# Kernel tuning notes

Hardware: AMD Instinct MI355X
Metric: run time of the kernel (lower is better)

Reference implementation:

```python
import jax, jax.numpy as jnp
import numpy as np

DK = 64  # embedding_size / h = 1024 / 16


def setup_inputs() -> dict:
    key = jax.random.key(0)
    k1, k2, k3 = jax.random.split(key, 3)
    S = 8192
    return {
        "q": jax.random.normal(k1, (S, DK), dtype=jnp.float32),
        "k": jax.random.normal(k2, (S, DK), dtype=jnp.float32),
        "v": jax.random.normal(k3, (S, DK), dtype=jnp.float32),
    }


def reference(q, k, v):
    # scores: [S, S]; NOTE: source scales by 1/dk (not 1/sqrt(dk)) — kept faithful.
    qk = jnp.matmul(q, k.T) * (1.0 / DK)
    S = qk.shape[0]
    # causal mask: position (i, j) allowed iff i >= j (0 added), else -inf
    i = jnp.arange(S)[:, None]
    j = jnp.arange(S)[None, :]
    qk = jnp.where(i >= j, qk, -jnp.inf)
    attn = jax.nn.softmax(qk, axis=-1)
    return jnp.matmul(attn, v)
```

## Files before the change

### kernel.cpp

```cpp
#include <hip/hip_runtime.h>
#include <hip/hip_bf16.h>

#define S_LEN 8192
#define DKD   64
#define BM    64
#define BN    64
#define PAD   8
#define LDK   (DKD + PAD)

#define CHUNK 512
#define NC    (S_LEN / CHUNK)
#define NWORK 1088

#define WS_NEED ((size_t)2 * S_LEN * DKD * 2 + (size_t)NC * S_LEN * 4 + (size_t)NC * S_LEN * DKD * 2)

typedef __bf16 bf16x8 __attribute__((ext_vector_type(8)));
typedef float  f32x4  __attribute__((ext_vector_type(4)));
typedef unsigned short ushort8v __attribute__((ext_vector_type(8)));
typedef unsigned short ushort4v __attribute__((ext_vector_type(4)));

__device__ __forceinline__ unsigned short f2bf(float f) {
  union { float f; unsigned u; } v; v.f = f;
  unsigned u = v.u;
  return (unsigned short)((u + 0x7fffu + ((u >> 16) & 1u)) >> 16);
}
__device__ __forceinline__ float bf2f(unsigned short s) {
  union { unsigned u; float f; } v; v.u = ((unsigned)s) << 16;
  return v.f;
}
__device__ __forceinline__ unsigned pk2(float a, float b) {
  union { float f; unsigned u; } x, y; x.f = a; y.f = b;
  return ((x.u + 0x8000u) >> 16) | ((y.u + 0x8000u) & 0xffff0000u);
}
__device__ __forceinline__ bf16x8 q_frag8(const float* p, float sc) {
  float4 u = *(const float4*)p;
  float4 w = *(const float4*)(p + 4);
  union { ushort8v s; bf16x8 b; } r;
  r.s[0] = f2bf(u.x * sc); r.s[1] = f2bf(u.y * sc);
  r.s[2] = f2bf(u.z * sc); r.s[3] = f2bf(u.w * sc);
  r.s[4] = f2bf(w.x * sc); r.s[5] = f2bf(w.y * sc);
  r.s[6] = f2bf(w.z * sc); r.s[7] = f2bf(w.w * sc);
  return r.b;
}

__global__ __launch_bounds__(256) void precompute(const float* __restrict__ k,
                                                  const float* __restrict__ v,
                                                  unsigned short* __restrict__ Ff) {
  __shared__ unsigned short Ls[64][72];
  const int b = blockIdx.x, tid = threadIdx.x;
  unsigned short* tb = Ff + ((size_t)b << 13);

#pragma unroll
  for (int j = 0; j < 4; ++j) {
    int vi = tid + j * 256;
    int row = vi >> 4, c4 = vi & 15;
    float4 x = *(const float4*)(v + ((size_t)(b * 64 + row)) * DKD + c4 * 4);
    Ls[row][c4 * 4 + 0] = f2bf(x.x);
    Ls[row][c4 * 4 + 1] = f2bf(x.y);
    Ls[row][c4 * 4 + 2] = f2bf(x.z);
    Ls[row][c4 * 4 + 3] = f2bf(x.w);
  }

#pragma unroll
  for (int j = 0; j < 2; ++j) {
    int idx = tid + j * 256;
    int f = idx >> 6, lane = idx & 63;
    int col = lane & 15, quad = lane >> 4;
    int t = f >> 1, c = f & 1;
    const float* src = k + ((size_t)(b * 64 + 16 * t + col)) * DKD + c * 32 + quad * 8;
    union { ushort8v s; bf16x8 bb; } r;
    r.bb = q_frag8(src, 1.0f);
    *(ushort8v*)(tb + (size_t)(f * 64 + lane) * 8) = r.s;
  }
  __syncthreads();

#pragma unroll
  for (int j = 0; j < 2; ++j) {
    int idx = tid + j * 256;
    int f8 = idx >> 6, lane = idx & 63;
    int col = lane & 15, quad = lane >> 4;
    int dt = f8 >> 1, c = f8 & 1;
    int d = 16 * dt + col;
    ushort8v o;
#pragma unroll
    for (int j2 = 0; j2 < 8; ++j2) {
      int kk = c * 32 + quad * 8 + j2;
      int s = (((kk & 7) >> 2) + 2 * (kk >> 5)) * 16 + (((kk >> 3) & 3) << 2) + (kk & 3);
      o[j2] = Ls[s][d];
    }
    *(ushort8v*)(tb + (size_t)((8 + f8) * 64 + lane) * 8) = o;
  }
}

__global__ __launch_bounds__(256) void attn_partial(const float* __restrict__ qg,
                                                    const unsigned short* __restrict__ Ff,
                                                    unsigned short* __restrict__ Opart,
                                                    float* __restrict__ l_ws) {
  const int w = blockIdx.x;
  int g = (int)((sqrtf((float)w + 1.0f) - 1.0f) * 0.5f);
  while (4 * (g + 1) * (g + 2) <= w) ++g;
  while (4 * g * (g + 1) > w) --g;
  const int r0  = w - 4 * g * (g + 1);
  const int qq  = r0 / (g + 1);
  const int qt  = 8 * g + qq;
  const int cch = r0 - qq * (g + 1);

  const int q0 = qt * BM, chunk0 = cch * CHUNK;
  const int n_kt = min(CHUNK / BN, qt - 8 * cch + 1);
  const int tile0 = chunk0 >> 6;

  const int tid = threadIdx.x, wave = tid >> 6, lane = tid & 63;
  const int col = lane & 15, quad = lane >> 4;

  const int qidx = q0 + wave * 16 + col;
  const float* qp = qg + (size_t)qidx * DKD;
  bf16x8 b0 = q_frag8(qp + quad * 8, 1.0f / 64.0f);
  bf16x8 b1 = q_frag8(qp + 32 + quad * 8, 1.0f / 64.0f);

  float lsum = 0.0f;
  f32x4 Of[4];
#pragma unroll
  for (int i = 0; i < 4; ++i) Of[i] = f32x4{0.0f, 0.0f, 0.0f, 0.0f};

  for (int it = 0; it < n_kt; ++it) {
    const unsigned short* tb = Ff + ((size_t)(tile0 + it) << 13);
    const int k0 = chunk0 + it * BN;

    bf16x8 kf[8];
#pragma unroll
    for (int f = 0; f < 8; ++f)
      kf[f] = *(const bf16x8*)(tb + (size_t)((f << 6) + lane) * 8);

    f32x4 Sf[4];
#pragma unroll
    for (int t = 0; t < 4; ++t) {
      f32x4 acc = f32x4{0.0f, 0.0f, 0.0f, 0.0f};
      acc = __builtin_amdgcn_mfma_f32_16x16x32_bf16(kf[2 * t], b0, acc, 0, 0, 0);
      acc = __builtin_amdgcn_mfma_f32_16x16x32_bf16(kf[2 * t + 1], b1, acc, 0, 0, 0);
      Sf[t] = acc;
    }

    bf16x8 vf[8];
#pragma unroll
    for (int f = 0; f < 8; ++f)
      vf[f] = *(const bf16x8*)(tb + (size_t)(((8 + f) << 6) + lane) * 8);

#pragma unroll
    for (int t = 0; t < 4; ++t) {
      int kb = k0 + t * 16 + quad * 4;
#pragma unroll
      for (int r = 0; r < 4; ++r) {
        float p = __expf(Sf[t][r]);
        p = (kb + r <= qidx) ? p : 0.0f;
        Sf[t][r] = p;
        lsum += p;
      }
    }

    union { unsigned u[4]; bf16x8 b; } pa0, pa1;
    pa0.u[0] = pk2(Sf[0][0], Sf[0][1]); pa0.u[1] = pk2(Sf[0][2], Sf[0][3]);
    pa0.u[2] = pk2(Sf[1][0], Sf[1][1]); pa0.u[3] = pk2(Sf[1][2], Sf[1][3]);
    pa1.u[0] = pk2(Sf[2][0], Sf[2][1]); pa1.u[1] = pk2(Sf[2][2], Sf[2][3]);
    pa1.u[2] = pk2(Sf[3][0], Sf[3][1]); pa1.u[3] = pk2(Sf[3][2], Sf[3][3]);

#pragma unroll
    for (int dt = 0; dt < 4; ++dt) {
      Of[dt] = __builtin_amdgcn_mfma_f32_16x16x32_bf16(pa0.b, vf[2 * dt], Of[dt], 0, 0, 0);
      Of[dt] = __builtin_amdgcn_mfma_f32_16x16x32_bf16(pa1.b, vf[2 * dt + 1], Of[dt], 0, 0, 0);
    }
  }

  lsum += __shfl_xor(lsum, 16);
  lsum += __shfl_xor(lsum, 32);
  if (lane < 16)
    l_ws[cch * S_LEN + q0 + wave * 16 + lane] = lsum;

#pragma unroll
  for (int r = 0; r < 4; ++r) {
    int rowg = q0 + wave * 16 + quad * 4 + r;
    uint2 o2;
    o2.x = pk2(Of[0][r], Of[1][r]);
    o2.y = pk2(Of[2][r], Of[3][r]);
    *(uint2*)(Opart + ((size_t)cch * S_LEN + rowg) * DKD + col * 4) = o2;
  }
}

__global__ __launch_bounds__(256) void attn_merge(const unsigned short* __restrict__ Opart,
                                                  const float* __restrict__ l_ws,
                                                  float* __restrict__ out) {
  int idx = blockIdx.x * 256 + threadIdx.x;
  int row = idx >> 3, m = idx & 7;
  int nc = (row >> 9) + 1;

  float acc[8] = {0, 0, 0, 0, 0, 0, 0, 0};
  float L = 0.0f;
  for (int c = 0; c < nc; ++c) {
    L += l_ws[c * S_LEN + row];
    ushort8v o = *(const ushort8v*)(Opart + ((size_t)c * S_LEN + row) * DKD + m * 8);
#pragma unroll
    for (int j = 0; j < 8; ++j) acc[j] += bf2f(o[j]);
  }
  float inv = 1.0f / L;
#pragma unroll
  for (int j0 = 0; j0 < 4; ++j0) {
    float2 w2 = { acc[j0] * inv, acc[j0 + 4] * inv };
    *(float2*)(out + (size_t)row * DKD + 16 * j0 + 2 * m) = w2;
  }
}

__global__ __launch_bounds__(128) void attn_fwd(const float* __restrict__ qg,
                                                const float* __restrict__ kg,
                                                const float* __restrict__ vg,
                                                float* __restrict__ out) {
  __shared__ __align__(16) unsigned short Qs[32][LDK];
  __shared__ __align__(16) unsigned short Ksh[BN][LDK];
  __shared__ __align__(16) unsigned short Vt[DKD][LDK];
  __shared__ __align__(16) unsigned short Ps[2][16][LDK];

  const int tid = threadIdx.x, wave = tid >> 6, lane = tid & 63;
  const int col = lane & 15, quad = lane >> 4;
  const int q0 = blockIdx.x * 32;

#pragma unroll
  for (int r = 0; r < 4; ++r) {
    int vi = tid + r * 128;
    int row = vi >> 4, c4 = vi & 15;
    if (row < 32) {
      float4 val = *(const float4*)(qg + (size_t)(q0 + row) * DKD + c4 * 4);
      Qs[row][c4 * 4 + 0] = f2bf(val.x);
      Qs[row][c4 * 4 + 1] = f2bf(val.y);
      Qs[row][c4 * 4 + 2] = f2bf(val.z);
      Qs[row][c4 * 4 + 3] = f2bf(val.w);
    }
  }

  float m_run[4], l_run[4];
  f32x4 Of[4];
#pragma unroll
  for (int i = 0; i < 4; ++i) {
    m_run[i] = -1e30f; l_run[i] = 0.0f;
    Of[i] = f32x4{0.0f, 0.0f, 0.0f, 0.0f};
  }

  const int n_tiles = (q0 + 31) / BN + 1;
  for (int it = 0; it < n_tiles; ++it) {
    __syncthreads();
    const int k0 = it * BN;
#pragma unroll
    for (int r = 0; r < 8; ++r) {
      int vi = tid + r * 128;
      int row = vi >> 4, c4 = vi & 15;
      float4 kv = *(const float4*)(kg + (size_t)(k0 + row) * DKD + c4 * 4);
      Ksh[row][c4 * 4 + 0] = f2bf(kv.x);
      Ksh[row][c4 * 4 + 1] = f2bf(kv.y);
      Ksh[row][c4 * 4 + 2] = f2bf(kv.z);
      Ksh[row][c4 * 4 + 3] = f2bf(kv.w);
      float4 vv = *(const float4*)(vg + (size_t)(k0 + row) * DKD + c4 * 4);
      Vt[c4 * 4 + 0][row] = f2bf(vv.x);
      Vt[c4 * 4 + 1][row] = f2bf(vv.y);
      Vt[c4 * 4 + 2][row] = f2bf(vv.z);
      Vt[c4 * 4 + 3][row] = f2bf(vv.w);
    }
    __syncthreads();

    f32x4 Sf[4];
    const unsigned short* qrow = &Qs[wave * 16 + col][0];
#pragma unroll
    for (int t = 0; t < 4; ++t) {
      f32x4 acc = f32x4{0.0f, 0.0f, 0.0f, 0.0f};
#pragma unroll
      for (int c = 0; c < 2; ++c) {
        bf16x8 a = *(const bf16x8*)(qrow + c * 32 + quad * 8);
        bf16x8 b = *(const bf16x8*)(&Ksh[t * 16 + col][c * 32 + quad * 8]);
        acc = __builtin_amdgcn_mfma_f32_16x16x32_bf16(a, b, acc, 0, 0, 0);
      }
      Sf[t] = acc;
    }

    const float scale = 1.0f / 64.0f;
    float rmax[4] = {-1e30f, -1e30f, -1e30f, -1e30f};
#pragma unroll
    for (int t = 0; t < 4; ++t) {
      int kidx = k0 + t * 16 + col;
#pragma unroll
      for (int r = 0; r < 4; ++r) {
        int qidx = q0 + wave * 16 + quad * 4 + r;
        float s = Sf[t][r] * scale;
        s = (kidx <= qidx) ? s : -1e30f;
        Sf[t][r] = s;
        rmax[r] = fmaxf(rmax[r], s);
      }
    }
#pragma unroll
    for (int off = 1; off <= 8; off <<= 1)
#pragma unroll
      for (int r = 0; r < 4; ++r)
        rmax[r] = fmaxf(rmax[r], __shfl_xor(rmax[r], off));

    float alpha[4], rsum[4];
#pragma unroll
    for (int r = 0; r < 4; ++r) {
      float mn = fmaxf(m_run[r], rmax[r]);
      alpha[r] = __expf(m_run[r] - mn);
      m_run[r] = mn;
      rsum[r] = 0.0f;
    }
#pragma unroll
    for (int t = 0; t < 4; ++t)
#pragma unroll
      for (int r = 0; r < 4; ++r) {
        float p = __expf(Sf[t][r] - m_run[r]);
        Sf[t][r] = p;
        rsum[r] += p;
      }
#pragma unroll
    for (int off = 1; off <= 8; off <<= 1)
#pragma unroll
      for (int r = 0; r < 4; ++r)
        rsum[r] += __shfl_xor(rsum[r], off);
#pragma unroll
    for (int r = 0; r < 4; ++r)
      l_run[r] = l_run[r] * alpha[r] + rsum[r];
#pragma unroll
    for (int dt = 0; dt < 4; ++dt)
#pragma unroll
      for (int r = 0; r < 4; ++r)
        Of[dt][r] *= alpha[r];

#pragma unroll
    for (int t = 0; t < 4; ++t)
#pragma unroll
      for (int r = 0; r < 4; ++r)
        Ps[wave][quad * 4 + r][t * 16 + col] = f2bf(Sf[t][r]);
    __syncthreads();

    const unsigned short* prow = &Ps[wave][col][0];
#pragma unroll
    for (int dt = 0; dt < 4; ++dt) {
#pragma unroll
      for (int c = 0; c < 2; ++c) {
        bf16x8 a = *(const bf16x8*)(prow + c * 32 + quad * 8);
        bf16x8 b = *(const bf16x8*)(&Vt[dt * 16 + col][c * 32 + quad * 8]);
        Of[dt] = __builtin_amdgcn_mfma_f32_16x16x32_bf16(a, b, Of[dt], 0, 0, 0);
      }
    }
  }

#pragma unroll
  for (int r = 0; r < 4; ++r) {
    float inv = 1.0f / l_run[r];
    int qrow_g = q0 + wave * 16 + quad * 4 + r;
#pragma unroll
    for (int dt = 0; dt < 4; ++dt)
      out[(size_t)qrow_g * DKD + dt * 16 + col] = Of[dt][r] * inv;
  }
}

extern "C" void kernel_launch(void* const* d_in, const int* in_sizes, int n_in,
                              void* d_out, int out_size, void* d_ws, size_t ws_size,
                              hipStream_t stream) {
  const float* q = (const float*)d_in[0];
  const float* k = (const float*)d_in[1];
  const float* v = (const float*)d_in[2];
  float* out = (float*)d_out;

  if (ws_size >= WS_NEED) {
    unsigned short* Ff    = (unsigned short*)d_ws;
    float* l_ws           = (float*)(Ff + (size_t)2 * S_LEN * DKD);
    unsigned short* Opart = (unsigned short*)(l_ws + (size_t)NC * S_LEN);

    hipLaunchKernelGGL(precompute, dim3(S_LEN / 64), dim3(256), 0, stream, k, v, Ff);
    hipLaunchKernelGGL(attn_partial, dim3(NWORK), dim3(256), 0, stream,
                       q, Ff, Opart, l_ws);
    hipLaunchKernelGGL(attn_merge, dim3(S_LEN * 8 / 256), dim3(256), 0, stream,
                       Opart, l_ws, out);
  } else {
    hipLaunchKernelGGL(attn_fwd, dim3(S_LEN / 32), dim3(128), 0, stream, q, k, v, out);
  }
}
```

Before: 94.79 us.

## Double query tile per block and stage K/V tiles through LDS with async loads

```diff
diff --git a/kernel.cpp b/kernel.cpp
--- a/kernel.cpp
+++ b/kernel.cpp
@@ -3,14 +3,14 @@
 
 #define S_LEN 8192
 #define DKD   64
-#define BM    64
+#define BM    128
 #define BN    64
 #define PAD   8
 #define LDK   (DKD + PAD)
 
 #define CHUNK 512
 #define NC    (S_LEN / CHUNK)
-#define NWORK 1088
+#define NWORK 544
 
 #define WS_NEED ((size_t)2 * S_LEN * DKD * 2 + (size_t)NC * S_LEN * 4 + (size_t)NC * S_LEN * DKD * 2)
 
@@ -18,6 +18,9 @@
 typedef float  f32x4  __attribute__((ext_vector_type(4)));
 typedef unsigned short ushort8v __attribute__((ext_vector_type(8)));
 typedef unsigned short ushort4v __attribute__((ext_vector_type(4)));
+
+typedef __attribute__((address_space(3))) unsigned int lds_uint;
+typedef const __attribute__((address_space(1))) unsigned int glb_uint;
 
 __device__ __forceinline__ unsigned short f2bf(float f) {
   union { float f; unsigned u; } v; v.f = f;
@@ -92,96 +95,143 @@
   }
 }
 
+__device__ __forceinline__ void stage_tile(const unsigned short* tb,
+                                           unsigned short* dst,
+                                           int wave) {
+#pragma unroll
+  for (int p = 0; p < 4; ++p) {
+    const int seg = p * 4 + wave;
+    __builtin_amdgcn_global_load_lds(
+        (glb_uint*)(tb + ((size_t)seg << 9) + (size_t)(threadIdx.x & 63) * 8),
+        (lds_uint*)(dst + ((size_t)seg << 9)),
+        16, 0, 0);
+  }
+}
+
 __global__ __launch_bounds__(256) void attn_partial(const float* __restrict__ qg,
                                                     const unsigned short* __restrict__ Ff,
                                                     unsigned short* __restrict__ Opart,
                                                     float* __restrict__ l_ws) {
-  const int w = blockIdx.x;
-  int g = (int)((sqrtf((float)w + 1.0f) - 1.0f) * 0.5f);
-  while (4 * (g + 1) * (g + 2) <= w) ++g;
-  while (4 * g * (g + 1) > w) --g;
-  const int r0  = w - 4 * g * (g + 1);
+  const int wr = (NWORK - 1) - blockIdx.x;
+  int g = (int)((sqrtf(2.0f * wr + 1.0f) - 1.0f) * 0.5f);
+  while (2 * (g + 1) * (g + 2) <= wr) ++g;
+  while (2 * g * (g + 1) > wr) --g;
+  const int r0  = wr - 2 * g * (g + 1);
   const int qq  = r0 / (g + 1);
-  const int qt  = 8 * g + qq;
+  const int qt  = 4 * g + qq;
   const int cch = r0 - qq * (g + 1);
 
   const int q0 = qt * BM, chunk0 = cch * CHUNK;
-  const int n_kt = min(CHUNK / BN, qt - 8 * cch + 1);
-  const int tile0 = chunk0 >> 6;
+  const int n_kt = min(CHUNK / BN, 2 * qt + 2 - 8 * cch);
+  const int tile0 = cch * 8;
+
+  __shared__ __align__(16) unsigned short Buf[2][8192];
 
   const int tid = threadIdx.x, wave = tid >> 6, lane = tid & 63;
   const int col = lane & 15, quad = lane >> 4;
 
-  const int qidx = q0 + wave * 16 + col;
-  const float* qp = qg + (size_t)qidx * DKD;
-  bf16x8 b0 = q_frag8(qp + quad * 8, 1.0f / 64.0f);
-  bf16x8 b1 = q_frag8(qp + 32 + quad * 8, 1.0f / 64.0f);
-
-  float lsum = 0.0f;
-  f32x4 Of[4];
-#pragma unroll
-  for (int i = 0; i < 4; ++i) Of[i] = f32x4{0.0f, 0.0f, 0.0f, 0.0f};
+  const int base0 = q0 + wave * 32;
+  const int qi0 = base0 + col, qi1 = base0 + 16 + col;
+  bf16x8 b0g0 = q_frag8(qg + (size_t)qi0 * DKD + quad * 8, 1.0f / 64.0f);
+  bf16x8 b1g0 = q_frag8(qg + (size_t)qi0 * DKD + 32 + quad * 8, 1.0f / 64.0f);
+  bf16x8 b0g1 = q_frag8(qg + (size_t)qi1 * DKD + quad * 8, 1.0f / 64.0f);
+  bf16x8 b1g1 = q_frag8(qg + (size_t)qi1 * DKD + 32 + quad * 8, 1.0f / 64.0f);
+
+  float ls0 = 0.0f, ls1 = 0.0f;
+  f32x4 Of0[4], Of1[4];
+#pragma unroll
+  for (int i = 0; i < 4; ++i) {
+    Of0[i] = f32x4{0.0f, 0.0f, 0.0f, 0.0f};
+    Of1[i] = f32x4{0.0f, 0.0f, 0.0f, 0.0f};
+  }
+
+  stage_tile(Ff + ((size_t)tile0 << 13), &Buf[0][0], wave);
+  __syncthreads();
 
   for (int it = 0; it < n_kt; ++it) {
-    const unsigned short* tb = Ff + ((size_t)(tile0 + it) << 13);
+    if (it + 1 < n_kt)
+      stage_tile(Ff + ((size_t)(tile0 + it + 1) << 13), &Buf[(it + 1) & 1][0], wave);
+
+    const unsigned short* B = &Buf[it & 1][0];
     const int k0 = chunk0 + it * BN;
 
     bf16x8 kf[8];
 #pragma unroll
     for (int f = 0; f < 8; ++f)
-      kf[f] = *(const bf16x8*)(tb + (size_t)((f << 6) + lane) * 8);
-
-    f32x4 Sf[4];
+      kf[f] = *(const bf16x8*)(B + (size_t)((f << 6) + lane) * 8);
+
+    f32x4 S0[4], S1[4];
 #pragma unroll
     for (int t = 0; t < 4; ++t) {
-      f32x4 acc = f32x4{0.0f, 0.0f, 0.0f, 0.0f};
-      acc = __builtin_amdgcn_mfma_f32_16x16x32_bf16(kf[2 * t], b0, acc, 0, 0, 0);
-      acc = __builtin_amdgcn_mfma_f32_16x16x32_bf16(kf[2 * t + 1], b1, acc, 0, 0, 0);
-      Sf[t] = acc;
+      f32x4 a0 = f32x4{0.0f, 0.0f, 0.0f, 0.0f};
+      a0 = __builtin_amdgcn_mfma_f32_16x16x32_bf16(kf[2 * t], b0g0, a0, 0, 0, 0);
+      a0 = __builtin_amdgcn_mfma_f32_16x16x32_bf16(kf[2 * t + 1], b1g0, a0, 0, 0, 0);
+      S0[t] = a0;
+      f32x4 a1 = f32x4{0.0f, 0.0f, 0.0f, 0.0f};
+      a1 = __builtin_amdgcn_mfma_f32_16x16x32_bf16(kf[2 * t], b0g1, a1, 0, 0, 0);
+      a1 = __builtin_amdgcn_mfma_f32_16x16x32_bf16(kf[2 * t + 1], b1g1, a1, 0, 0, 0);
+      S1[t] = a1;
     }
 
     bf16x8 vf[8];
 #pragma unroll
     for (int f = 0; f < 8; ++f)
-      vf[f] = *(const bf16x8*)(tb + (size_t)(((8 + f) << 6) + lane) * 8);
+      vf[f] = *(const bf16x8*)(B + (size_t)(((8 + f) << 6) + lane) * 8);
 
 #pragma unroll
     for (int t = 0; t < 4; ++t) {
       int kb = k0 + t * 16 + quad * 4;
 #pragma unroll
       for (int r = 0; r < 4; ++r) {
-        float p = __expf(Sf[t][r]);
-        p = (kb + r <= qidx) ? p : 0.0f;
-        Sf[t][r] = p;
-        lsum += p;
+        float p0 = __expf(S0[t][r]);
+        p0 = (kb + r <= qi0) ? p0 : 0.0f;
+        S0[t][r] = p0; ls0 += p0;
+        float p1 = __expf(S1[t][r]);
+        p1 = (kb + r <= qi1) ? p1 : 0.0f;
+        S1[t][r] = p1; ls1 += p1;
       }
     }
 
-    union { unsigned u[4]; bf16x8 b; } pa0, pa1;
-    pa0.u[0] = pk2(Sf[0][0], Sf[0][1]); pa0.u[1] = pk2(Sf[0][2], Sf[0][3]);
-    pa0.u[2] = pk2(Sf[1][0], Sf[1][1]); pa0.u[3] = pk2(Sf[1][2], Sf[1][3]);
-    pa1.u[0] = pk2(Sf[2][0], Sf[2][1]); pa1.u[1] = pk2(Sf[2][2], Sf[2][3]);
-    pa1.u[2] = pk2(Sf[3][0], Sf[3][1]); pa1.u[3] = pk2(Sf[3][2], Sf[3][3]);
+    union { unsigned u[4]; bf16x8 b; } pa0g0, pa1g0, pa0g1, pa1g1;
+    pa0g0.u[0] = pk2(S0[0][0], S0[0][1]); pa0g0.u[1] = pk2(S0[0][2], S0[0][3]);
+    pa0g0.u[2] = pk2(S0[1][0], S0[1][1]); pa0g0.u[3] = pk2(S0[1][2], S0[1][3]);
+    pa1g0.u[0] = pk2(S0[2][0], S0[2][1]); pa1g0.u[1] = pk2(S0[2][2], S0[2][3]);
+    pa1g0.u[2] = pk2(S0[3][0], S0[3][1]); pa1g0.u[3] = pk2(S0[3][2], S0[3][3]);
+    pa0g1.u[0] = pk2(S1[0][0], S1[0][1]); pa0g1.u[1] = pk2(S1[0][2], S1[0][3]);
+    pa0g1.u[2] = pk2(S1[1][0], S1[1][1]); pa0g1.u[3] = pk2(S1[1][2], S1[1][3]);
+    pa1g1.u[0] = pk2(S1[2][0], S1[2][1]); pa1g1.u[1] = pk2(S1[2][2], S1[2][3]);
+    pa1g1.u[2] = pk2(S1[3][0], S1[3][1]); pa1g1.u[3] = pk2(S1[3][2], S1[3][3]);
 
 #pragma unroll
     for (int dt = 0; dt < 4; ++dt) {
-      Of[dt] = __builtin_amdgcn_mfma_f32_16x16x32_bf16(pa0.b, vf[2 * dt], Of[dt], 0, 0, 0);
-      Of[dt] = __builtin_amdgcn_mfma_f32_16x16x32_bf16(pa1.b, vf[2 * dt + 1], Of[dt], 0, 0, 0);
-    }
-  }
-
-  lsum += __shfl_xor(lsum, 16);
-  lsum += __shfl_xor(lsum, 32);
-  if (lane < 16)
-    l_ws[cch * S_LEN + q0 + wave * 16 + lane] = lsum;
+      Of0[dt] = __builtin_amdgcn_mfma_f32_16x16x32_bf16(pa0g0.b, vf[2 * dt], Of0[dt], 0, 0, 0);
+      Of0[dt] = __builtin_amdgcn_mfma_f32_16x16x32_bf16(pa1g0.b, vf[2 * dt + 1], Of0[dt], 0, 0, 0);
+      Of1[dt] = __builtin_amdgcn_mfma_f32_16x16x32_bf16(pa0g1.b, vf[2 * dt], Of1[dt], 0, 0, 0);
+      Of1[dt] = __builtin_amdgcn_mfma_f32_16x16x32_bf16(pa1g1.b, vf[2 * dt + 1], Of1[dt], 0, 0, 0);
+    }
+
+    __syncthreads();
+  }
+
+  ls0 += __shfl_xor(ls0, 16); ls0 += __shfl_xor(ls0, 32);
+  ls1 += __shfl_xor(ls1, 16); ls1 += __shfl_xor(ls1, 32);
+  if (lane < 16) {
+    l_ws[cch * S_LEN + base0 + lane] = ls0;
+    l_ws[cch * S_LEN + base0 + 16 + lane] = ls1;
+  }
 
 #pragma unroll
   for (int r = 0; r < 4; ++r) {
-    int rowg = q0 + wave * 16 + quad * 4 + r;
+    int rg0 = base0 + quad * 4 + r;
     uint2 o2;
-    o2.x = pk2(Of[0][r], Of[1][r]);
-    o2.y = pk2(Of[2][r], Of[3][r]);
-    *(uint2*)(Opart + ((size_t)cch * S_LEN + rowg) * DKD + col * 4) = o2;
+    o2.x = pk2(Of0[0][r], Of0[1][r]);
+    o2.y = pk2(Of0[2][r], Of0[3][r]);
+    *(uint2*)(Opart + ((size_t)cch * S_LEN + rg0) * DKD + col * 4) = o2;
+    int rg1 = base0 + 16 + quad * 4 + r;
+    uint2 p2;
+    p2.x = pk2(Of1[0][r], Of1[1][r]);
+    p2.y = pk2(Of1[2][r], Of1[3][r]);
+    *(uint2*)(Opart + ((size_t)cch * S_LEN + rg1) * DKD + col * 4) = p2;
   }
 }
 
```

Result: faster. 92.11 us (-2.8%).

## Double-buffer K/V tiles in LDS via async global_load_lds and reverse block order

Applied to the files above, without the earlier changes.

```diff
diff --git a/kernel.cpp b/kernel.cpp
--- a/kernel.cpp
+++ b/kernel.cpp
@@ -18,6 +18,9 @@
 typedef float  f32x4  __attribute__((ext_vector_type(4)));
 typedef unsigned short ushort8v __attribute__((ext_vector_type(8)));
 typedef unsigned short ushort4v __attribute__((ext_vector_type(4)));
+
+typedef __attribute__((address_space(3))) unsigned int lds_uint;
+typedef const __attribute__((address_space(1))) unsigned int glb_uint;
 
 __device__ __forceinline__ unsigned short f2bf(float f) {
   union { float f; unsigned u; } v; v.f = f;
@@ -92,22 +95,37 @@
   }
 }
 
+__device__ __forceinline__ void stage_tile(const unsigned short* tb,
+                                           unsigned short* dst,
+                                           int wave) {
+#pragma unroll
+  for (int p = 0; p < 4; ++p) {
+    const int seg = p * 4 + wave;
+    __builtin_amdgcn_global_load_lds(
+        (glb_uint*)(tb + ((size_t)seg << 9) + (size_t)(threadIdx.x & 63) * 8),
+        (lds_uint*)(dst + ((size_t)seg << 9)),
+        16, 0, 0);
+  }
+}
+
 __global__ __launch_bounds__(256) void attn_partial(const float* __restrict__ qg,
                                                     const unsigned short* __restrict__ Ff,
                                                     unsigned short* __restrict__ Opart,
                                                     float* __restrict__ l_ws) {
-  const int w = blockIdx.x;
-  int g = (int)((sqrtf((float)w + 1.0f) - 1.0f) * 0.5f);
-  while (4 * (g + 1) * (g + 2) <= w) ++g;
-  while (4 * g * (g + 1) > w) --g;
-  const int r0  = w - 4 * g * (g + 1);
+  const int wr = (NWORK - 1) - blockIdx.x;
+  int g = (int)((sqrtf((float)wr + 1.0f) - 1.0f) * 0.5f);
+  while (4 * (g + 1) * (g + 2) <= wr) ++g;
+  while (4 * g * (g + 1) > wr) --g;
+  const int r0  = wr - 4 * g * (g + 1);
   const int qq  = r0 / (g + 1);
   const int qt  = 8 * g + qq;
   const int cch = r0 - qq * (g + 1);
 
   const int q0 = qt * BM, chunk0 = cch * CHUNK;
   const int n_kt = min(CHUNK / BN, qt - 8 * cch + 1);
-  const int tile0 = chunk0 >> 6;
+  const int tile0 = cch * 8;
+
+  __shared__ __align__(16) unsigned short Buf[2][8192];
 
   const int tid = threadIdx.x, wave = tid >> 6, lane = tid & 63;
   const int col = lane & 15, quad = lane >> 4;
@@ -122,14 +140,20 @@
 #pragma unroll
   for (int i = 0; i < 4; ++i) Of[i] = f32x4{0.0f, 0.0f, 0.0f, 0.0f};
 
+  stage_tile(Ff + ((size_t)tile0 << 13), &Buf[0][0], wave);
+  __syncthreads();
+
   for (int it = 0; it < n_kt; ++it) {
-    const unsigned short* tb = Ff + ((size_t)(tile0 + it) << 13);
+    if (it + 1 < n_kt)
+      stage_tile(Ff + ((size_t)(tile0 + it + 1) << 13), &Buf[(it + 1) & 1][0], wave);
+
+    const unsigned short* B = &Buf[it & 1][0];
     const int k0 = chunk0 + it * BN;
 
     bf16x8 kf[8];
 #pragma unroll
     for (int f = 0; f < 8; ++f)
-      kf[f] = *(const bf16x8*)(tb + (size_t)((f << 6) + lane) * 8);
+      kf[f] = *(const bf16x8*)(B + (size_t)((f << 6) + lane) * 8);
 
     f32x4 Sf[4];
 #pragma unroll
@@ -143,7 +167,7 @@
     bf16x8 vf[8];
 #pragma unroll
     for (int f = 0; f < 8; ++f)
-      vf[f] = *(const bf16x8*)(tb + (size_t)(((8 + f) << 6) + lane) * 8);
+      vf[f] = *(const bf16x8*)(B + (size_t)(((8 + f) << 6) + lane) * 8);
 
 #pragma unroll
     for (int t = 0; t < 4; ++t) {
@@ -168,6 +192,8 @@
       Of[dt] = __builtin_amdgcn_mfma_f32_16x16x32_bf16(pa0.b, vf[2 * dt], Of[dt], 0, 0, 0);
       Of[dt] = __builtin_amdgcn_mfma_f32_16x16x32_bf16(pa1.b, vf[2 * dt + 1], Of[dt], 0, 0, 0);
     }
+
+    __syncthreads();
   }
 
   lsum += __shfl_xor(lsum, 16);
```

Result: faster. 88.51 us, median of 2 (-6.6%).
